# Performance work log

Measured on AMD Instinct MI355X. Metric: run time of the kernel, lower is better.

The kernel has to match this reference:

```python
import jax, jax.numpy as jnp
import numpy as np

EPS = 1e-4
SLOPE = 0.01
NFFT = 512
HOP = 256
CH_IN = 8
CH_H = 64
FREQ = NFFT // 2 + 1
LEN = 48000
BATCH = 2


def hann(n):
    return (0.5 - 0.5 * jnp.cos(2.0 * np.pi * jnp.arange(n) / n)).astype(jnp.float32)


def stft(x):
    # x: (B, C, L) -> (B, 2, C, F, T)  (torch.stft: center=True, reflect pad, hann window)
    pad = NFFT // 2
    xp = jnp.pad(x, ((0, 0), (0, 0), (pad, pad)), mode='reflect')
    T = 1 + x.shape[-1] // HOP
    idx = jnp.arange(T)[:, None] * HOP + jnp.arange(NFFT)[None, :]
    frames = xp[..., idx] * hann(NFFT)            # (B, C, T, NFFT)
    sp = jnp.fft.rfft(frames, axis=-1)            # (B, C, T, F)
    sp = jnp.swapaxes(sp, -1, -2)                 # (B, C, F, T)
    return jnp.stack([sp.real, sp.imag], axis=1).astype(jnp.float32)


def istft(re, im, length):
    # re, im: (B, C, F, T) -> (B, C, length) via windowed overlap-add
    sp = jnp.swapaxes(re + 1j * im, -1, -2)       # (B, C, T, F)
    win = hann(NFFT)
    frames = jnp.fft.irfft(sp, n=NFFT, axis=-1) * win
    pad = NFFT // 2
    total = length + 2 * pad
    T = frames.shape[-2]
    idx = jnp.arange(T)[:, None] * HOP + jnp.arange(NFFT)[None, :]
    out = jnp.zeros(frames.shape[:-2] + (total,), frames.dtype).at[..., idx].add(frames)
    wsum = jnp.zeros((total,), frames.dtype).at[idx].add(jnp.broadcast_to(win ** 2, (T, NFFT)))
    return (out / jnp.maximum(wsum, 1e-11))[..., pad:pad + length]


def conv2d(x, w, b, padT=0):
    y = jax.lax.conv_general_dilated(x, w, (1, 1), ((0, 0), (padT, padT)),
                                     dimension_numbers=('NCHW', 'OIHW', 'NCHW'))
    return y + b[None, :, None, None]


def cconv(x, w, b, padT=0):
    # complex conv on x: (B,2,C,F,T); w: (2,O,C,kf,kt) = [W_real, W_imag]; b: (2,O)
    r = conv2d(x[:, 0], w[0], b[0], padT) - conv2d(x[:, 1], w[1], b[1], padT)
    i = conv2d(x[:, 1], w[0], b[0], padT) + conv2d(x[:, 0], w[1], b[1], padT)
    return jnp.stack([r, i], axis=1)


def modExp(x, m=5.0):
    em = float(np.exp(m))
    return jnp.where(x > m, (x - m) * em + em, jnp.exp(jnp.minimum(x, m)))


def cExp(t):
    e = modExp(t[:, 0]) - 1.0
    return jnp.stack([e * jnp.cos(t[:, 1] - 1.0), e * jnp.sin(t[:, 1] - 1.0)], axis=1)


def snap(x):
    x = jnp.where((x >= 0) & (x < EPS), EPS, x)
    return jnp.where((x < 0) & (x > -EPS), -EPS, x)


def cLog(t):
    re = snap(t[:, 0])
    im = snap(t[:, 1])
    real = jnp.log(jnp.sqrt(im ** 2 + re ** 2 + EPS ** 2) + 1.0)
    imag = jnp.arctan(im / re)
    return jnp.stack([real, imag], axis=1)


def cMul(a, b):
    r = a[:, 0] * b[:, 0] - a[:, 1] * b[:, 1]
    i = a[:, 0] * b[:, 1] + a[:, 1] * b[:, 0]
    return jnp.stack([r, i], axis=1)


def trelu(t, tr, b):
    nr = t[:, 0] * tr[0, 0] + t[:, 1] * tr[0, 1] + b[0]
    ni = t[:, 0] * tr[1, 0] + t[:, 1] * tr[1, 1] + b[1]
    return jnp.stack([jax.nn.leaky_relu(nr, SLOPE), jax.nn.leaky_relu(ni, SLOPE)], axis=1)


def tgate(t, tr, b):
    gr = jax.nn.sigmoid(t[:, 0] * tr[0, 0] + t[:, 1] * tr[0, 1] + b[0])
    gi = jax.nn.sigmoid(t[:, 0] * tr[1, 0] + t[:, 1] * tr[1, 1] + b[1])
    return gr * gi + (1.0 - gr) * (1.0 - gi)


def perm(t):
    return jnp.transpose(t, (0, 1, 3, 2, 4))


def lrelu(x):
    return jax.nn.leaky_relu(x, SLOPE)


def forward(mix, fs_w, fs_b, fr_w, fr_b, c1r_w, c1r_b, c1i_w, c1i_b, c1_w, c1_b,
            c2r_w, c2r_b, c2i_w, c2i_b, c2_w, c2_b, a1_t, a1_b, a2_t, a2_b,
            c3r_w, c3r_b, c3i_w, c3i_b, c3_w, c3_b, c4r_w, c4r_b, c4i_w, c4i_b,
            c4_w, c4_b, a3_t, a3_b, a4_t, a4_b, f1_w, f1_b, f2_w, f2_b,
            cw_w, cw_b, fg_t, fg_b):
    ts = perm(cconv(perm(stft(mix)), fs_w, fs_b))      # (B,2,C,F,T)
    # ---- branch 1 ----
    tl = cLog(ts)
    tl = jnp.stack([conv2d(tl[:, 0], c1r_w, c1r_b), conv2d(tl[:, 1], c1r_w, c1r_b)], 1)
    tl = jnp.stack([conv2d(lrelu(tl[:, 0]), c1i_w, c1i_b), conv2d(tl[:, 1], c1i_w, c1i_b)], 1)
    tl = trelu(cExp(tl), a1_t, a1_b)
    t = cconv(tl, c1_w, c1_b)
    tl = cLog(t)
    tl = jnp.stack([conv2d(tl[:, 0], c2r_w, c2r_b, 7), conv2d(tl[:, 1], c2r_w, c2r_b, 7)], 1)[..., :-7]
    tl = jnp.stack([conv2d(lrelu(tl[:, 0]), c2i_w, c2i_b, 7), conv2d(tl[:, 1], c2i_w, c2i_b, 7)], 1)[..., :-7]
    tl = cExp(tl)
    tl1 = tl
    tc = cconv(ts, c2_w, c2_b, 7)[..., :-7]
    t = trelu(cMul(tl, tc), a2_t, a2_b)
    t = cconv(t, f1_w, f1_b)
    td1 = jnp.sum(ts - t, axis=2, keepdims=True) / ts.shape[2]
    # ---- branch 2 ----
    tl = cLog(ts)
    tl = jnp.stack([conv2d(tl[:, 0], c3r_w, c3r_b), conv2d(tl[:, 1], c3r_w, c3r_b)], 1)
    tl = jnp.stack([conv2d(lrelu(tl[:, 0]), c3i_w, c3i_b), conv2d(tl[:, 1], c3i_w, c3i_b)], 1)
    tl = trelu(cExp(tl), a3_t, a3_b)
    t = cconv(tl, c3_w, c3_b)
    tl = cLog(t)
    tl = jnp.stack([conv2d(tl[:, 0], c4r_w, c4r_b, 7), conv2d(tl[:, 1], c4r_w, c4r_b, 7)], 1)[..., :-7]
    tl = jnp.stack([conv2d(lrelu(tl[:, 0]), c4i_w, c4i_b, 7), conv2d(tl[:, 1], c4i_w, c4i_b, 7)], 1)[..., :-7]
    tl = cExp(tl)
    tc = cconv(ts, c4_w, c4_b, 7)[..., :-7]
    t = trelu(cMul(tl, tc), a4_t, a4_b)
    td2 = cconv(t, f2_w, f2_b)                         # (B,2,1,F,T)
    # ---- fuse ----
    f = cconv(jnp.concatenate([tl1, tl], axis=2), cw_w, cw_b)
    f = tgate(f, fg_t, fg_b)[:, None]                  # (B,1,1,F,T)
    td = td1 * f + td2 * (1.0 - f)
    t = perm(cconv(perm(td), fr_w, fr_b))
    return istft(t[:, 0], t[:, 1], LEN)                # (B,1,LEN)


def setup_inputs() -> dict:
    ks = iter(jax.random.split(jax.random.key(0), 64))
    def rn(shape, s=0.05):
        return s * jax.random.normal(next(ks), shape, jnp.float32)
    F, C, H = FREQ, CH_IN, CH_H
    inp = {
        'mix': jax.random.normal(next(ks), (BATCH, C, LEN), jnp.float32),
        'fs_w': rn((2, F, F, 1, 1)), 'fs_b': rn((2, F), 0.01),
        'fr_w': rn((2, F, F, 1, 1)), 'fr_b': rn((2, F), 0.01),
        'c1r_w': rn((H, C, 1, 1)), 'c1r_b': rn((H,), 0.01),
        'c1i_w': rn((H, H, 1, 1)), 'c1i_b': rn((H,), 0.01),
        'c1_w': rn((2, H, H, 1, 1)), 'c1_b': rn((2, H), 0.01),
        'c2r_w': rn((H, H, 1, 8)), 'c2r_b': rn((H,), 0.01),
        'c2i_w': rn((H, H, 1, 8)), 'c2i_b': rn((H,), 0.01),
        'c2_w': rn((2, H, C, 1, 8)), 'c2_b': rn((2, H), 0.01),
        'a1_t': rn((2, 2, H, F, 1), 0.5), 'a1_b': rn((2, H, F, 1), 0.5),
        'a2_t': rn((2, 2, H, F, 1), 0.5), 'a2_b': rn((2, H, F, 1), 0.5),
        'c3r_w': rn((H, C, 1, 1)), 'c3r_b': rn((H,), 0.01),
        'c3i_w': rn((H, H, 1, 1)), 'c3i_b': rn((H,), 0.01),
        'c3_w': rn((2, H, H, 1, 1)), 'c3_b': rn((2, H), 0.01),
        'c4r_w': rn((H, H, 1, 8)), 'c4r_b': rn((H,), 0.01),
        'c4i_w': rn((H, H, 1, 8)), 'c4i_b': rn((H,), 0.01),
        'c4_w': rn((2, H, C, 1, 8)), 'c4_b': rn((2, H), 0.01),
        'a3_t': rn((2, 2, H, F, 1), 0.5), 'a3_b': rn((2, H, F, 1), 0.5),
        'a4_t': rn((2, 2, H, F, 1), 0.5), 'a4_b': rn((2, H, F, 1), 0.5),
        'f1_w': rn((2, C, H, 1, 1)), 'f1_b': rn((2, C), 0.01),
        'f2_w': rn((2, 1, H, 1, 1)), 'f2_b': rn((2, 1), 0.01),
        'cw_w': rn((2, 1, 2 * H, 1, 1)), 'cw_b': rn((2, 1), 0.01),
        'fg_t': rn((2, 2, 1, F, 1), 0.5), 'fg_b': rn((2, 1, F, 1), 0.5),
    }
    return inp


def reference(mix, fs_w, fs_b, fr_w, fr_b, c1r_w, c1r_b, c1i_w, c1i_b, c1_w, c1_b,
              c2r_w, c2r_b, c2i_w, c2i_b, c2_w, c2_b, a1_t, a1_b, a2_t, a2_b,
              c3r_w, c3r_b, c3i_w, c3i_b, c3_w, c3_b, c4r_w, c4r_b, c4i_w, c4i_b,
              c4_w, c4_b, a3_t, a3_b, a4_t, a4_b, f1_w, f1_b, f2_w, f2_b,
              cw_w, cw_b, fg_t, fg_b):
    return forward(mix, fs_w, fs_b, fr_w, fr_b, c1r_w, c1r_b, c1i_w, c1i_b, c1_w, c1_b,
                   c2r_w, c2r_b, c2i_w, c2i_b, c2_w, c2_b, a1_t, a1_b, a2_t, a2_b,
                   c3r_w, c3r_b, c3i_w, c3i_b, c3_w, c3_b, c4r_w, c4r_b, c4i_w, c4i_b,
                   c4_w, c4_b, a3_t, a3_b, a4_t, a4_b, f1_w, f1_b, f2_w, f2_b,
                   cw_w, cw_b, fg_t, fg_b)
```

## Files before the change

kernel.cpp:

```cpp
#include <hip/hip_runtime.h>
#include <math.h>

#define DEV __device__ __forceinline__

constexpr int B_   = 2;
constexpr int C_IN = 8;
constexpr int H_   = 64;
constexpr int F_   = 257;
constexpr int T_   = 188;
constexpr int TW   = 96;
constexpr int NFFT = 512;
constexpr int HOP  = 256;
constexpr int LEN  = 48000;
constexpr int PADL = 256;
constexpr int FT   = F_ * T_;
constexpr float EPSV  = 1e-4f;
constexpr float SLOPEV = 0.01f;
constexpr float PI2 = 6.283185307179586f;

typedef __attribute__((ext_vector_type(8))) short short8;
typedef __attribute__((ext_vector_type(4))) short short4v;
typedef __attribute__((ext_vector_type(4))) float float4v;

DEV float lrelu_f(float x) { return x > 0.f ? x : SLOPEV * x; }
DEV float snap_f(float x) {
  if (x >= 0.f && x < EPSV) return EPSV;
  if (x < 0.f && x > -EPSV) return -EPSV;
  return x;
}
DEV float fast_atan(float z) {
  float az = fabsf(z);
  float u = az > 1.f ? __builtin_amdgcn_rcpf(az) : az;
  float u2 = u * u;
  float p = -0.01172120f;
  p = p * u2 + 0.05265332f;
  p = p * u2 - 0.11643287f;
  p = p * u2 + 0.19354346f;
  p = p * u2 - 0.33262347f;
  p = p * u2 + 0.99997726f;
  float r = p * u;
  if (az > 1.f) r = 1.5707963267948966f - r;
  return z < 0.f ? -r : r;
}
DEV float modexp_f(float x) {
  const float em = 148.4131591025766f;
  return x > 5.f ? (x - 5.f) * em + em : __expf(x);
}
DEV void cexp_f(float tr, float ti, float& er, float& ei) {
  float e = modexp_f(tr) - 1.f;
  float a = ti - 1.f;
  er = e * __cosf(a); ei = e * __sinf(a);
}
DEV float sigmoid_f(float x) { return 1.f / (1.f + __expf(-x)); }

DEV short f2bf(float x) {
  unsigned u = __float_as_uint(x);
  unsigned r = (u + 0x7fffu + ((u >> 16) & 1u)) >> 16;
  return (short)r;
}
DEV float bf2f(short h) {
  return __uint_as_float(((unsigned)(unsigned short)h) << 16);
}

__global__ void k_mixsplit(const float* __restrict__ x, short* __restrict__ hi,
                           short* __restrict__ lo) {
  int i = blockIdx.x * 256 + threadIdx.x;
  if (i >= B_ * C_IN * LEN / 4) return;
  float4v v = *(const float4v*)(x + (size_t)i * 4);
  short4v h, l;
  #pragma unroll
  for (int j = 0; j < 4; ++j) {
    h[j] = f2bf(v[j]);
    l[j] = f2bf(v[j] - bf2f(h[j]));
  }
  *(short4v*)(hi + (size_t)i * 4) = h;
  *(short4v*)(lo + (size_t)i * 4) = l;
}

__global__ __launch_bounds__(256) void k_mixdft(const float* __restrict__ W,
                                                short* __restrict__ wpk) {
  constexpr int MT = 33;
  __shared__ float wr_s[F_], wi_s[F_];
  int m = blockIdx.x;
  int k = blockIdx.y * 256 + threadIdx.x;
  int po = m >= F_;
  int fo = m - po * F_;
  if (m < 2 * F_) {
    for (int i = threadIdx.x; i < F_; i += 256) {
      wr_s[i] = W[fo * F_ + i];
      wi_s[i] = W[F_ * F_ + fo * F_ + i];
    }
  }
  __syncthreads();
  float val = 0.f;
  if (m < 2 * F_) {
    float sd, cd;
    sincosf((PI2 / NFFT) * k, &sd, &cd);
    float cs = 1.f, sn = 0.f;
    float ar = 0.f, ai = 0.f;
    for (int fi = 0; fi < F_; ++fi) {
      float wrv = wr_s[fi], wiv = wi_s[fi];
      ar += wrv * cs + wiv * sn;
      ai += wiv * cs - wrv * sn;
      float t2 = cs * cd - sn * sd;
      sn = sn * cd + cs * sd;
      cs = t2;
    }
    float win = 0.5f - 0.5f * cd;
    val = (po ? ai : ar) * win;
  }
  int mtg = m >> 4;
  int lane2 = ((k >> 3) & 3) * 16 + (m & 15);
  int s = k >> 5;
  int j = k & 7;
  short hi = f2bf(val);
  short lo = f2bf(val - bf2f(hi));
  wpk[(((0 * 16 + s) * MT + mtg) * 64 + lane2) * 8 + j] = hi;
  wpk[(((16 + s) * MT + mtg) * 64 + lane2) * 8 + j] = lo;
}

constexpr int TWS = 48;
__global__ __launch_bounds__(256) void k_stftmix(
    const short* __restrict__ mhi, const short* __restrict__ mlo,
    const short* __restrict__ wpk, const float* __restrict__ bias,
    float* __restrict__ Y) {
  constexpr int PITCH = 136;
  constexpr int MT = 33;
  __shared__ short xs_hi[TWS * PITCH];
  __shared__ short xs_lo[TWS * PITCH];
  int mg = blockIdx.x;
  int bc = blockIdx.y;
  int b = bc >> 3, c = bc & 7;
  int t0 = blockIdx.z * TWS;
  int tid = threadIdx.x;
  int lane = tid & 63;
  int wv = __builtin_amdgcn_readfirstlane(tid >> 6);
  int mtg = mg * 4 + wv;
  int q = lane >> 4;
  int n = lane & 15;

  const short* mh_ = mhi + (size_t)(b * C_IN + c) * LEN;
  const short* ml_ = mlo + (size_t)(b * C_IN + c) * LEN;

  float4v acc[3];
  #pragma unroll
  for (int nt = 0; nt < 3; ++nt) acc[nt] = (float4v)(0.f);

  const short8* wp = (const short8*)wpk;
  for (int round = 0; round < 4; ++round) {
    if (round) __syncthreads();
    for (int i = tid; i < TWS * 16; i += 256) {
      int tl = i >> 4, u = i & 15;
      int kk0 = u * 8;
      int t = t0 + tl;
      int g0 = t * HOP + round * 128 + kk0 - PADL;
      short8 h, l;
      if (t < T_ && g0 >= 0 && g0 + 7 < LEN) {
        h = *(const short8*)(mh_ + g0);
        l = *(const short8*)(ml_ + g0);
      } else {
        #pragma unroll
        for (int j = 0; j < 8; ++j) {
          short hv = 0, lv = 0;
          if (t < T_) {
            int g = g0 + j;
            if (g < 0) g = -g;
            if (g >= LEN) g = 2 * LEN - 2 - g;
            hv = mh_[g]; lv = ml_[g];
          }
          h[j] = hv; l[j] = lv;
        }
      }
      *(short8*)&xs_hi[tl * PITCH + kk0] = h;
      *(short8*)&xs_lo[tl * PITCH + kk0] = l;
    }
    __syncthreads();
    #pragma unroll
    for (int s2 = 0; s2 < 4; ++s2) {
      int s = round * 4 + s2;
      short8 Ah, Al;
      if (mtg < MT) {
        Ah = wp[((0 * 16 + s) * MT + mtg) * 64 + lane];
        Al = wp[((16 + s) * MT + mtg) * 64 + lane];
      }
      short8 Bh[3], Bl[3];
      #pragma unroll
      for (int nt = 0; nt < 3; ++nt) {
        int off = (nt * 16 + n) * PITCH + s2 * 32 + q * 8;
        Bh[nt] = *(const short8*)&xs_hi[off];
        Bl[nt] = *(const short8*)&xs_lo[off];
      }
      if (mtg < MT) {
        #pragma unroll
        for (int nt = 0; nt < 3; ++nt) {
          acc[nt] = __builtin_amdgcn_mfma_f32_16x16x32_bf16(Ah, Bh[nt], acc[nt], 0, 0, 0);
          acc[nt] = __builtin_amdgcn_mfma_f32_16x16x32_bf16(Ah, Bl[nt], acc[nt], 0, 0, 0);
          acc[nt] = __builtin_amdgcn_mfma_f32_16x16x32_bf16(Al, Bh[nt], acc[nt], 0, 0, 0);
        }
      }
    }
  }

  if (mtg < MT) {
    #pragma unroll
    for (int nt = 0; nt < 3; ++nt) {
      int t = t0 + nt * 16 + n;
      if (t >= T_) continue;
      #pragma unroll
      for (int r = 0; r < 4; ++r) {
        int m = mtg * 16 + q * 4 + r;
        if (m >= 2 * F_) continue;
        int po = m >= F_;
        int fo = m - po * F_;
        float badd = po ? bias[fo] + bias[F_ + fo] : bias[fo] - bias[F_ + fo];
        Y[((size_t)((b * 2 + po) * C_IN + c)) * FT + fo * T_ + t] = acc[nt][r] + badd;
      }
    }
  }
}

template<int CH>
__global__ void k_fmix(const float* __restrict__ X, const float* __restrict__ W,
                       const float* __restrict__ bias, float* __restrict__ Y) {
  int fo = blockIdx.x;
  int bc = blockIdx.y; int c = bc % CH; int b = bc / CH;
  int t = threadIdx.x;
  if (t >= T_) return;
  const float* wr = W + fo * F_;
  const float* wi = W + F_ * F_ + fo * F_;
  const float* xr = X + ((b * 2 + 0) * CH + c) * FT + t;
  const float* xi = X + ((b * 2 + 1) * CH + c) * FT + t;
  float ar = 0.f, ai = 0.f;
  for (int fi = 0; fi < F_; ++fi) {
    float wrv = wr[fi], wiv = wi[fi];
    float xrv = xr[fi * T_], xiv = xi[fi * T_];
    ar += wrv * xrv - wiv * xiv;
    ai += wrv * xiv + wiv * xrv;
  }
  float br = bias[fo], bi = bias[F_ + fo];
  Y[((b * 2 + 0) * CH + c) * FT + fo * T_ + t] = ar + br - bi;
  Y[((b * 2 + 1) * CH + c) * FT + fo * T_ + t] = ai + br + bi;
}

template<int CIN, int K>
DEV void repack_real_body(const float* __restrict__ W, short* __restrict__ wpk, int i) {
  constexpr int CC = (CIN >= 32) ? (CIN / 32) : 1;
  constexpr int NSTEP = (CIN * K + 31) / 32;
  int total = 2 * NSTEP * 4 * 64 * 8;
  if (i >= total) return;
  int j = i & 7;
  int lane = (i >> 3) & 63;
  int mt = (i >> 9) & 3;
  int s = (i >> 11) % NSTEP;
  int split = i / (NSTEP * 2048);
  int q = lane >> 4;
  int m = mt * 16 + (lane & 15);
  int tap = s / CC;
  int c = (s % CC) * 32 + q * 8 + j;
  float w = 0.f;
  if (c < CIN && tap < K) w = W[(m * CIN + c) * K + tap];
  short hi = f2bf(w);
  wpk[i] = split ? f2bf(w - bf2f(hi)) : hi;
}

template<int CIN2, int COUT2, int K>
DEV void repack_cplx_body(const float* __restrict__ W, short* __restrict__ wpk, int i) {
  constexpr int CIN = CIN2 / 2, COUT = COUT2 / 2;
  constexpr int NSTEP = CIN2 * K / 32;
  constexpr int MT = (COUT2 + 15) / 16;
  int total = 2 * NSTEP * MT * 64 * 8;
  if (i >= total) return;
  int j = i & 7;
  int lane = (i >> 3) & 63;
  int idx = i >> 9;
  int mt = idx % MT; idx /= MT;
  int s = idx % NSTEP;
  int split = idx / NSTEP;
  int q = lane >> 4;
  int m = mt * 16 + (lane & 15);
  int tap, pi, ci;
  if constexpr (CIN2 == 128) {
    tap = 0;
    int cs = s * 32 + q * 8 + j;
    int half = cs / 64, r = cs % 64;
    ci = half * 32 + r / 2;
    pi = r & 1;
  } else {
    tap = s * 2 + (q >> 1);
    int cs = (q & 1) * 8 + j;
    pi = cs / CIN;
    ci = cs % CIN;
  }
  float w = 0.f;
  if (m < COUT2) {
    int po = m / COUT, ho = m % COUT;
    float wr = W[((0 * COUT + ho) * CIN + ci) * K + tap];
    float wi = W[((1 * COUT + ho) * CIN + ci) * K + tap];
    w = (po == pi) ? wr : (po == 0 ? -wi : wi);
  }
  short hi = f2bf(w);
  wpk[i] = split ? f2bf(w - bf2f(hi)) : hi;
}

__global__ __launch_bounds__(256) void k_repack_all(
    const float* c1r_w, const float* c1i_w, const float* c2r_w, const float* c2i_w,
    const float* c3r_w, const float* c3i_w, const float* c4r_w, const float* c4i_w,
    const float* c1_w, const float* c2_w, const float* c3_w, const float* c4_w,
    const float* f1_w, const float* f2_w,
    short* o0, short* o1, short* o2, short* o3, short* o4, short* o5, short* o6,
    short* o7, short* o8, short* o9, short* o10, short* o11, short* o12, short* o13) {
  int i = blockIdx.x * 256 + threadIdx.x;
  switch (blockIdx.y) {
    case 0:  repack_real_body<C_IN, 1>(c1r_w, o0, i); break;
    case 1:  repack_real_body<H_,   1>(c1i_w, o1, i); break;
    case 2:  repack_real_body<H_,   8>(c2r_w, o2, i); break;
    case 3:  repack_real_body<H_,   8>(c2i_w, o3, i); break;
    case 4:  repack_real_body<C_IN, 1>(c3r_w, o4, i); break;
    case 5:  repack_real_body<H_,   1>(c3i_w, o5, i); break;
    case 6:  repack_real_body<H_,   8>(c4r_w, o6, i); break;
    case 7:  repack_real_body<H_,   8>(c4i_w, o7, i); break;
    case 8:  repack_cplx_body<128, 128, 1>(c1_w, o8, i); break;
    case 9:  repack_cplx_body<16,  128, 8>(c2_w, o9, i); break;
    case 10: repack_cplx_body<128, 128, 1>(c3_w, o10, i); break;
    case 11: repack_cplx_body<16,  128, 8>(c4_w, o11, i); break;
    case 12: repack_cplx_body<128, 16,  1>(f1_w, o12, i); break;
    case 13: repack_cplx_body<128, 2,   1>(f2_w, o13, i); break;
  }
}

template<int CIN, int K, int PRO>
__global__ __launch_bounds__(256) void k_conv_mfma(
    const float* __restrict__ X, const short* __restrict__ wpk,
    const float* __restrict__ bias, float* __restrict__ Y) {
  constexpr int CC = (CIN >= 32) ? (CIN / 32) : 1;
  constexpr int NSTEP = (CIN * K + 31) / 32;
  constexpr int PITCH = 72;
  constexpr int ROWS = TW + (K - 1);
  __shared__ short xs_hi[ROWS * PITCH];
  __shared__ short xs_lo[ROWS * PITCH];
  int f = blockIdx.x;
  int bp = blockIdx.y; int p = bp & 1; int b = bp >> 1;
  int t0 = blockIdx.z * TW;
  int tid = threadIdx.x;

  for (int i = tid; i < ROWS * PITCH; i += 256) { xs_hi[i] = 0; xs_lo[i] = 0; }
  __syncthreads();

  const float* Xr_ = X + (size_t)((b * 2 + 0) * CIN) * FT + f * T_;
  const float* Xi_ = X + (size_t)((b * 2 + 1) * CIN) * FT + f * T_;
  const float* Xp  = X + (size_t)((b * 2 + p) * CIN) * FT + f * T_;
  for (int i = tid; i < CIN * ROWS; i += 256) {
    int c = i / ROWS, rr = i % ROWS;
    int t = t0 + rr - (K - 1);
    if (t < 0 || t >= T_) continue;
    float v;
    if (PRO == 2) {
      float re = snap_f(Xr_[c * FT + t]);
      float im = snap_f(Xi_[c * FT + t]);
      v = (p == 0) ? __logf(sqrtf(im * im + re * re + EPSV * EPSV) + 1.f)
                   : fast_atan(im / re);
    } else {
      v = Xp[c * FT + t];
      if (PRO == 1 && p == 0) v = lrelu_f(v);
    }
    short hi = f2bf(v);
    short lo = f2bf(v - bf2f(hi));
    xs_hi[rr * PITCH + c] = hi;
    xs_lo[rr * PITCH + c] = lo;
  }
  __syncthreads();

  int lane = tid & 63;
  int wv = __builtin_amdgcn_readfirstlane(tid >> 6);
  int mh = wv >> 1;
  int tc = wv & 1;
  int q = lane >> 4;
  int n = lane & 15;
  int wbase = tc * 48;

  float4v acc[2][3];
  #pragma unroll
  for (int mt = 0; mt < 2; ++mt)
    #pragma unroll
    for (int nt = 0; nt < 3; ++nt) acc[mt][nt] = (float4v)(0.f);

  const short8* wp = (const short8*)wpk;
  #pragma unroll
  for (int s = 0; s < NSTEP; ++s) {
    int tap = s / CC;
    int c0 = (s % CC) * 32;
    short8 Ah[2], Al[2];
    #pragma unroll
    for (int mt = 0; mt < 2; ++mt) {
      int mtg = mh * 2 + mt;
      Ah[mt] = wp[((0 * NSTEP + s) * 4 + mtg) * 64 + lane];
      Al[mt] = wp[((1 * NSTEP + s) * 4 + mtg) * 64 + lane];
    }
    short8 Bh[3], Bl[3];
    #pragma unroll
    for (int nt = 0; nt < 3; ++nt) {
      int off = (wbase + nt * 16 + n + tap) * PITCH + c0 + q * 8;
      Bh[nt] = *(const short8*)&xs_hi[off];
      Bl[nt] = *(const short8*)&xs_lo[off];
    }
    #pragma unroll
    for (int mt = 0; mt < 2; ++mt) {
      #pragma unroll
      for (int nt = 0; nt < 3; ++nt) {
        acc[mt][nt] = __builtin_amdgcn_mfma_f32_16x16x32_bf16(Ah[mt], Bh[nt], acc[mt][nt], 0, 0, 0);
        acc[mt][nt] = __builtin_amdgcn_mfma_f32_16x16x32_bf16(Ah[mt], Bl[nt], acc[mt][nt], 0, 0, 0);
        acc[mt][nt] = __builtin_amdgcn_mfma_f32_16x16x32_bf16(Al[mt], Bh[nt], acc[mt][nt], 0, 0, 0);
      }
    }
  }

  float* Yp = Y + (size_t)((b * 2 + p) * H_) * FT + f * T_;
  #pragma unroll
  for (int nt = 0; nt < 3; ++nt) {
    int t = t0 + wbase + nt * 16 + n;
    if (t >= T_) continue;
    #pragma unroll
    for (int mt = 0; mt < 2; ++mt) {
      #pragma unroll
      for (int r = 0; r < 4; ++r) {
        int h = (mh * 2 + mt) * 16 + q * 4 + r;
        Yp[h * FT + t] = acc[mt][nt][r] + bias[h];
      }
    }
  }
}

template<int COUT2, int PRO>
__global__ __launch_bounds__(256) void k_cconv128(
    const float* __restrict__ X0, const float* __restrict__ X1,
    const short* __restrict__ wpk,
    const float* __restrict__ at, const float* __restrict__ ab,
    const float* __restrict__ bias, float* __restrict__ Y) {
  constexpr int MT = (COUT2 + 15) / 16;
  constexpr int MTW = (MT > 4) ? 4 : MT;
  constexpr int COUT = COUT2 / 2;
  constexpr int NSTEP = 4;
  constexpr int PITCH = 72;
  __shared__ short xs_hi[TW * PITCH];
  __shared__ short xs_lo[TW * PITCH];
  __shared__ float coef[6][64];
  int f = blockIdx.x;
  int b = blockIdx.y;
  int t0 = blockIdx.z * TW;
  int tid = threadIdx.x;
  int lane = tid & 63;
  int wv = __builtin_amdgcn_readfirstlane(tid >> 6);
  int mh = wv >> 1;
  int tc = wv & 1;
  int q = lane >> 4;
  int n = lane & 15;
  int wbase = tc * 48;

  if (tid < 64) {
    int h = tid;
    coef[0][h] = at[(0 * H_ + h) * F_ + f];
    coef[1][h] = at[(1 * H_ + h) * F_ + f];
    coef[2][h] = at[(2 * H_ + h) * F_ + f];
    coef[3][h] = at[(3 * H_ + h) * F_ + f];
    coef[4][h] = ab[h * F_ + f];
    coef[5][h] = ab[(H_ + h) * F_ + f];
  }
  for (int i = tid; i < TW * PITCH; i += 256) { xs_hi[i] = 0; xs_lo[i] = 0; }

  const float* b0r = X0 + (size_t)((b * 2 + 0) * H_) * FT + f * T_;
  const float* b0i = X0 + (size_t)((b * 2 + 1) * H_) * FT + f * T_;
  const float* b1r = X1 + (size_t)((b * 2 + 0) * H_) * FT + f * T_;
  const float* b1i = X1 + (size_t)((b * 2 + 1) * H_) * FT + f * T_;

  float4v acc[MTW][3];
  #pragma unroll
  for (int mt = 0; mt < MTW; ++mt)
    #pragma unroll
    for (int nt = 0; nt < 3; ++nt) acc[mt][nt] = (float4v)(0.f);

  const short8* wp = (const short8*)wpk;
  for (int half = 0; half < 2; ++half) {
    __syncthreads();
    for (int i = tid; i < 32 * TW; i += 256) {
      int hh = i / TW, tl = i % TW;
      int t = t0 + tl;
      if (t >= T_) continue;
      int h = half * 32 + hh;
      float xr = b0r[h * FT + t], xi = b0i[h * FT + t];
      float vr, vi;
      if (PRO == 1) {
        float er, ei;
        cexp_f(xr, xi, er, ei);
        vr = lrelu_f(er * coef[0][h] + ei * coef[1][h] + coef[4][h]);
        vi = lrelu_f(er * coef[2][h] + ei * coef[3][h] + coef[5][h]);
      } else {
        float yr = b1r[h * FT + t], yi = b1i[h * FT + t];
        float mr = xr * yr - xi * yi;
        float mi = xr * yi + xi * yr;
        vr = lrelu_f(mr * coef[0][h] + mi * coef[1][h] + coef[4][h]);
        vi = lrelu_f(mr * coef[2][h] + mi * coef[3][h] + coef[5][h]);
      }
      int cs0 = hh * 2, cs1 = hh * 2 + 1;
      short hr = f2bf(vr), hi2 = f2bf(vi);
      xs_hi[tl * PITCH + cs0] = hr;
      xs_lo[tl * PITCH + cs0] = f2bf(vr - bf2f(hr));
      xs_hi[tl * PITCH + cs1] = hi2;
      xs_lo[tl * PITCH + cs1] = f2bf(vi - bf2f(hi2));
    }
    __syncthreads();
    #pragma unroll
    for (int s2 = 0; s2 < 2; ++s2) {
      int s = half * 2 + s2;
      short8 Bh[3], Bl[3];
      #pragma unroll
      for (int nt = 0; nt < 3; ++nt) {
        int off = (wbase + nt * 16 + n) * PITCH + s2 * 32 + q * 8;
        Bh[nt] = *(const short8*)&xs_hi[off];
        Bl[nt] = *(const short8*)&xs_lo[off];
      }
      #pragma unroll
      for (int mt = 0; mt < MTW; ++mt) {
        int mtg = mh * 4 + mt;
        if (mtg >= MT) continue;
        short8 Ah = wp[((0 * NSTEP + s) * MT + mtg) * 64 + lane];
        short8 Al = wp[((1 * NSTEP + s) * MT + mtg) * 64 + lane];
        #pragma unroll
        for (int nt = 0; nt < 3; ++nt) {
          acc[mt][nt] = __builtin_amdgcn_mfma_f32_16x16x32_bf16(Ah, Bh[nt], acc[mt][nt], 0, 0, 0);
          acc[mt][nt] = __builtin_amdgcn_mfma_f32_16x16x32_bf16(Ah, Bl[nt], acc[mt][nt], 0, 0, 0);
          acc[mt][nt] = __builtin_amdgcn_mfma_f32_16x16x32_bf16(Al, Bh[nt], acc[mt][nt], 0, 0, 0);
        }
      }
    }
  }

  float* Yp = Y + (size_t)b * COUT2 * FT + f * T_;
  #pragma unroll
  for (int nt = 0; nt < 3; ++nt) {
    int t = t0 + wbase + nt * 16 + n;
    if (t >= T_) continue;
    #pragma unroll
    for (int mt = 0; mt < MTW; ++mt) {
      int mtg = mh * 4 + mt;
      if (mtg >= MT) continue;
      #pragma unroll
      for (int r = 0; r < 4; ++r) {
        int o2 = mtg * 16 + q * 4 + r;
        if (o2 >= COUT2) continue;
        int po = o2 / COUT, ho = o2 % COUT;
        float br = bias[ho], bi = bias[COUT + ho];
        float badd = (po == 0) ? br - bi : br + bi;
        Yp[o2 * FT + t] = acc[mt][nt][r] + badd;
      }
    }
  }
}

__global__ __launch_bounds__(256) void k_cconv16(
    const float* __restrict__ X, const short* __restrict__ wpk,
    const float* __restrict__ bias, float* __restrict__ Y) {
  constexpr int MT = 8, NSTEP = 4, PITCH = 24, ROWS = TW + 7, COUT = 64, COUT2 = 128;
  __shared__ short xs_hi[ROWS * PITCH];
  __shared__ short xs_lo[ROWS * PITCH];
  int f = blockIdx.x;
  int b = blockIdx.y;
  int t0 = blockIdx.z * TW;
  int tid = threadIdx.x;

  for (int i = tid; i < ROWS * PITCH; i += 256) { xs_hi[i] = 0; xs_lo[i] = 0; }
  __syncthreads();

  const float* Xp = X + (size_t)b * 16 * FT + f * T_;
  for (int i = tid; i < 16 * ROWS; i += 256) {
    int c = i / ROWS, rr = i % ROWS;
    int t = t0 + rr - 7;
    if (t < 0 || t >= T_) continue;
    float v = Xp[c * FT + t];
    short hi = f2bf(v);
    short lo = f2bf(v - bf2f(hi));
    xs_hi[rr * PITCH + c] = hi;
    xs_lo[rr * PITCH + c] = lo;
  }
  __syncthreads();

  int lane = tid & 63;
  int wv = __builtin_amdgcn_readfirstlane(tid >> 6);
  int mh = wv >> 1;
  int tc = wv & 1;
  int q = lane >> 4;
  int n = lane & 15;
  int wbase = tc * 48;

  float4v acc[4][3];
  #pragma unroll
  for (int mt = 0; mt < 4; ++mt)
    #pragma unroll
    for (int nt = 0; nt < 3; ++nt) acc[mt][nt] = (float4v)(0.f);

  const short8* wp = (const short8*)wpk;
  #pragma unroll
  for (int s = 0; s < NSTEP; ++s) {
    int tap = s * 2 + (q >> 1);
    int coff = (q & 1) * 8;
    short8 Bh[3], Bl[3];
    #pragma unroll
    for (int nt = 0; nt < 3; ++nt) {
      int off = (wbase + nt * 16 + n + tap) * PITCH + coff;
      Bh[nt] = *(const short8*)&xs_hi[off];
      Bl[nt] = *(const short8*)&xs_lo[off];
    }
    #pragma unroll
    for (int mt = 0; mt < 4; ++mt) {
      int mtg = mh * 4 + mt;
      short8 Ah = wp[((0 * NSTEP + s) * MT + mtg) * 64 + lane];
      short8 Al = wp[((1 * NSTEP + s) * MT + mtg) * 64 + lane];
      #pragma unroll
      for (int nt = 0; nt < 3; ++nt) {
        acc[mt][nt] = __builtin_amdgcn_mfma_f32_16x16x32_bf16(Ah, Bh[nt], acc[mt][nt], 0, 0, 0);
        acc[mt][nt] = __builtin_amdgcn_mfma_f32_16x16x32_bf16(Ah, Bl[nt], acc[mt][nt], 0, 0, 0);
        acc[mt][nt] = __builtin_amdgcn_mfma_f32_16x16x32_bf16(Al, Bh[nt], acc[mt][nt], 0, 0, 0);
      }
    }
  }

  float* Yp = Y + (size_t)b * COUT2 * FT + f * T_;
  #pragma unroll
  for (int nt = 0; nt < 3; ++nt) {
    int t = t0 + wbase + nt * 16 + n;
    if (t >= T_) continue;
    #pragma unroll
    for (int mt = 0; mt < 4; ++mt) {
      #pragma unroll
      for (int r = 0; r < 4; ++r) {
        int o2 = (mh * 4 + mt) * 16 + q * 4 + r;
        int po = o2 / COUT, ho = o2 % COUT;
        float br = bias[ho], bi = bias[COUT + ho];
        float badd = (po == 0) ? br - bi : br + bi;
        Yp[o2 * FT + t] = acc[mt][nt][r] + badd;
      }
    }
  }
}

__global__ void k_cexp(const float* __restrict__ X, float* __restrict__ Y) {
  int i = blockIdx.x * blockDim.x + threadIdx.x;
  if (i >= B_ * H_ * FT) return;
  int b = i / (H_ * FT);
  int r = i % (H_ * FT);
  int i0 = (b * 2) * H_ * FT + r;
  int i1 = i0 + H_ * FT;
  float er, ei;
  cexp_f(X[i0], X[i1], er, ei);
  Y[i0] = er;
  Y[i1] = ei;
}

__global__ void k_td1(const float* __restrict__ ts, const float* __restrict__ t8,
                      float* __restrict__ td1) {
  int i = blockIdx.x * blockDim.x + threadIdx.x;
  if (i >= B_ * 2 * FT) return;
  int bp = i / FT; int r = i % FT;
  const float* a = ts + bp * C_IN * FT + r;
  const float* c2 = t8 + bp * C_IN * FT + r;
  float acc = 0.f;
  #pragma unroll
  for (int c = 0; c < C_IN; ++c) acc += a[c * FT] - c2[c * FT];
  td1[i] = acc * (1.f / C_IN);
}

__global__ void k_fuse(const float* __restrict__ tl1, const float* __restrict__ tl2,
                       const float* __restrict__ td1, const float* __restrict__ td2,
                       const float* __restrict__ cw, const float* __restrict__ cwb,
                       const float* __restrict__ fgt, const float* __restrict__ fgb,
                       float* __restrict__ td) {
  int i = blockIdx.x * blockDim.x + threadIdx.x;
  if (i >= B_ * FT) return;
  int b = i / FT; int r = i % FT; int f = r / T_;
  const float* x1r = tl1 + (b * 2) * H_ * FT + r;
  const float* x1i = x1r + H_ * FT;
  const float* x2r = tl2 + (b * 2) * H_ * FT + r;
  const float* x2i = x2r + H_ * FT;
  float fr = 0.f, fi = 0.f;
  for (int c = 0; c < H_; ++c) {
    float w1r = cw[c], w2r = cw[H_ + c], w1i = cw[2 * H_ + c], w2i = cw[3 * H_ + c];
    float a1r = x1r[c * FT], a1i = x1i[c * FT];
    float a2r = x2r[c * FT], a2i = x2i[c * FT];
    fr += w1r * a1r - w1i * a1i + w2r * a2r - w2i * a2i;
    fi += w1r * a1i + w1i * a1r + w2r * a2i + w2i * a2r;
  }
  fr += cwb[0] - cwb[1];
  fi += cwb[0] + cwb[1];
  float t00 = fgt[f], t01 = fgt[F_ + f], t10 = fgt[2 * F_ + f], t11 = fgt[3 * F_ + f];
  float gr = sigmoid_f(fr * t00 + fi * t01 + fgb[f]);
  float gi = sigmoid_f(fr * t10 + fi * t11 + fgb[F_ + f]);
  float gg = gr * gi + (1.f - gr) * (1.f - gi);
  int i0 = (b * 2) * FT + r, i1 = i0 + FT;
  td[i0] = td1[i0] * gg + td2[i0] * (1.f - gg);
  td[i1] = td1[i1] * gg + td2[i1] * (1.f - gg);
}

__global__ __launch_bounds__(320) void k_iframes(const float* __restrict__ sp,
                                                 float* __restrict__ frames) {
  __shared__ float Xr[F_], Xi[F_];
  int blk = blockIdx.x;
  int t = blk % T_;
  int b = blk / T_;
  int tid = threadIdx.x;
  for (int i = tid; i < F_; i += 320) {
    Xr[i] = sp[(b * 2 + 0) * FT + i * T_ + t];
    Xi[i] = sp[(b * 2 + 1) * FT + i * T_ + t];
  }
  __syncthreads();
  int n = tid;
  if (n <= 256) {
    float sd, cd;
    sincosf((PI2 / NFFT) * n, &sd, &cd);
    float cs = cd, sn = sd;
    float ac = 0.f, as = 0.f;
    for (int f = 1; f < 256; ++f) {
      ac += Xr[f] * cs;
      as += Xi[f] * sn;
      float t2 = cs * cd - sn * sd;
      sn = sn * cd + cs * sd;
      cs = t2;
    }
    float base = Xr[0] + Xr[256] * (1.f - 2.f * (n & 1));
    float win = 0.5f - 0.5f * cd;
    float scale = win * (1.f / NFFT);
    float* fr = frames + (size_t)(b * T_ + t) * NFFT;
    fr[n] = (base + 2.f * ac - 2.f * as) * scale;
    if (n >= 1 && n <= 255)
      fr[NFFT - n] = (base + 2.f * ac + 2.f * as) * scale;
  }
}

__global__ void k_ola(const float* __restrict__ frames, float* __restrict__ out) {
  int i = blockIdx.x * blockDim.x + threadIdx.x;
  if (i >= B_ * LEN) return;
  int b = i / LEN; int j = i % LEN;
  int p = j + PADL;
  int t0 = p / HOP; int n0 = p - t0 * HOP;
  float acc = 0.f, wsum = 0.f;
  if (t0 < T_) {
    acc += frames[(b * T_ + t0) * NFFT + n0];
    float w = 0.5f - 0.5f * __cosf((PI2 / NFFT) * n0);
    wsum += w * w;
  }
  int t1 = t0 - 1, n1 = n0 + HOP;
  if (t1 >= 0 && t1 < T_) {
    acc += frames[(b * T_ + t1) * NFFT + n1];
    float w = 0.5f - 0.5f * __cosf((PI2 / NFFT) * n1);
    wsum += w * w;
  }
  out[i] = acc / fmaxf(wsum, 1e-11f);
}

extern "C" void kernel_launch(void* const* d_in, const int* in_sizes, int n_in,
                              void* d_out, int out_size, void* d_ws, size_t ws_size,
                              hipStream_t stream) {
  const float* mix   = (const float*)d_in[0];
  const float* fs_w  = (const float*)d_in[1];
  const float* fs_b  = (const float*)d_in[2];
  const float* fr_w  = (const float*)d_in[3];
  const float* fr_b  = (const float*)d_in[4];
  const float* c1r_w = (const float*)d_in[5];
  const float* c1r_b = (const float*)d_in[6];
  const float* c1i_w = (const float*)d_in[7];
  const float* c1i_b = (const float*)d_in[8];
  const float* c1_w  = (const float*)d_in[9];
  const float* c1_b  = (const float*)d_in[10];
  const float* c2r_w = (const float*)d_in[11];
  const float* c2r_b = (const float*)d_in[12];
  const float* c2i_w = (const float*)d_in[13];
  const float* c2i_b = (const float*)d_in[14];
  const float* c2_w  = (const float*)d_in[15];
  const float* c2_b  = (const float*)d_in[16];
  const float* a1_t  = (const float*)d_in[17];
  const float* a1_b  = (const float*)d_in[18];
  const float* a2_t  = (const float*)d_in[19];
  const float* a2_b  = (const float*)d_in[20];
  const float* c3r_w = (const float*)d_in[21];
  const float* c3r_b = (const float*)d_in[22];
  const float* c3i_w = (const float*)d_in[23];
  const float* c3i_b = (const float*)d_in[24];
  const float* c3_w  = (const float*)d_in[25];
  const float* c3_b  = (const float*)d_in[26];
  const float* c4r_w = (const float*)d_in[27];
  const float* c4r_b = (const float*)d_in[28];
  const float* c4i_w = (const float*)d_in[29];
  const float* c4i_b = (const float*)d_in[30];
  const float* c4_w  = (const float*)d_in[31];
  const float* c4_b  = (const float*)d_in[32];
  const float* a3_t  = (const float*)d_in[33];
  const float* a3_b  = (const float*)d_in[34];
  const float* a4_t  = (const float*)d_in[35];
  const float* a4_b  = (const float*)d_in[36];
  const float* f1_w  = (const float*)d_in[37];
  const float* f1_b  = (const float*)d_in[38];
  const float* f2_w  = (const float*)d_in[39];
  const float* f2_b  = (const float*)d_in[40];
  const float* cw_w  = (const float*)d_in[41];
  const float* cw_b  = (const float*)d_in[42];
  const float* fg_t  = (const float*)d_in[43];
  const float* fg_b  = (const float*)d_in[44];

  const size_t S8 = (size_t)B_ * 2 * C_IN * FT;
  const size_t SH = (size_t)B_ * 2 * H_ * FT;
  const size_t S1 = (size_t)B_ * 2 * FT;
  float* ws  = (float*)d_ws;
  float* ts0 = ws;
  float* ts  = ts0 + S8;
  float* A   = ts + S8;
  float* Bb  = A + SH;
  float* Cc  = Bb + SH;
  float* td1 = Cc + SH;
  float* td2 = td1 + S1;
  float* tdf = td2 + S1;
  float* tdr = tdf + S1;
  float* s8  = ts0;
  float* frames = ts0;

  short* wtail = (short*)(tdr + S1);
  constexpr int SZ_C8K1   = 2 * 1  * 4 * 64 * 8;
  constexpr int SZ_C64K1  = 2 * 2  * 4 * 64 * 8;
  constexpr int SZ_C64K8  = 2 * 16 * 4 * 64 * 8;
  constexpr int SZ_CC128  = 2 * 4  * 8 * 64 * 8;
  constexpr int SZ_CF     = 2 * 4  * 1 * 64 * 8;
  constexpr int SZ_SM     = 2 * 16 * 33 * 64 * 8;
  short* w_c1r = wtail;
  short* w_c1i = w_c1r + SZ_C8K1;
  short* w_c2r = w_c1i + SZ_C64K1;
  short* w_c2i = w_c2r + SZ_C64K8;
  short* w_c3r = w_c2i + SZ_C64K8;
  short* w_c3i = w_c3r + SZ_C8K1;
  short* w_c4r = w_c3i + SZ_C64K1;
  short* w_c4i = w_c4r + SZ_C64K8;
  short* w_cc1 = w_c4i + SZ_C64K8;
  short* w_cc2 = w_cc1 + SZ_CC128;
  short* w_cc3 = w_cc2 + SZ_CC128;
  short* w_cc4 = w_cc3 + SZ_CC128;
  short* w_cf1 = w_cc4 + SZ_CC128;
  short* w_cf2 = w_cf1 + SZ_CF;
  short* w_sm  = w_cf2 + SZ_CF;
  short* mhi   = w_sm + SZ_SM;
  short* mlo   = mhi + (size_t)B_ * C_IN * LEN;

  const int nH = B_ * H_ * FT;
  const int nP = B_ * FT;
  const dim3 rgrid(F_, B_ * 2, 2);
  const dim3 cgrid(F_, B_, 2);

  k_repack_all<<<dim3(256, 14), 256, 0, stream>>>(
      c1r_w, c1i_w, c2r_w, c2i_w, c3r_w, c3i_w, c4r_w, c4i_w,
      c1_w, c2_w, c3_w, c4_w, f1_w, f2_w,
      w_c1r, w_c1i, w_c2r, w_c2i, w_c3r, w_c3i, w_c4r, w_c4i,
      w_cc1, w_cc2, w_cc3, w_cc4, w_cf1, w_cf2);

  k_mixsplit<<<(B_ * C_IN * LEN / 4 + 255) / 256, 256, 0, stream>>>(mix, mhi, mlo);
  k_mixdft<<<dim3(528, 2), 256, 0, stream>>>(fs_w, w_sm);
  k_stftmix<<<dim3(9, 16, 4), 256, 0, stream>>>(mhi, mlo, w_sm, fs_b, ts);

  k_conv_mfma<C_IN, 1, 2><<<rgrid, 256, 0, stream>>>(ts, w_c1r, c1r_b, A);
  k_conv_mfma<H_, 1, 1><<<rgrid, 256, 0, stream>>>(A, w_c1i, c1i_b, Bb);
  k_cconv128<128, 1><<<cgrid, 256, 0, stream>>>(Bb, Bb, w_cc1, a1_t, a1_b, c1_b, A);
  k_conv_mfma<H_, 8, 2><<<rgrid, 256, 0, stream>>>(A, w_c2r, c2r_b, Bb);
  k_conv_mfma<H_, 8, 1><<<rgrid, 256, 0, stream>>>(Bb, w_c2i, c2i_b, A);
  k_cexp<<<(nH + 255) / 256, 256, 0, stream>>>(A, Bb);
  k_cconv16<<<cgrid, 256, 0, stream>>>(ts, w_cc2, c2_b, A);
  k_cconv128<16, 2><<<cgrid, 256, 0, stream>>>(Bb, A, w_cf1, a2_t, a2_b, f1_b, s8);
  k_td1<<<(B_ * 2 * FT + 255) / 256, 256, 0, stream>>>(ts, s8, td1);

  k_conv_mfma<C_IN, 1, 2><<<rgrid, 256, 0, stream>>>(ts, w_c3r, c3r_b, A);
  k_conv_mfma<H_, 1, 1><<<rgrid, 256, 0, stream>>>(A, w_c3i, c3i_b, Cc);
  k_cconv128<128, 1><<<cgrid, 256, 0, stream>>>(Cc, Cc, w_cc3, a3_t, a3_b, c3_b, A);
  k_conv_mfma<H_, 8, 2><<<rgrid, 256, 0, stream>>>(A, w_c4r, c4r_b, Cc);
  k_conv_mfma<H_, 8, 1><<<rgrid, 256, 0, stream>>>(Cc, w_c4i, c4i_b, A);
  k_cexp<<<(nH + 255) / 256, 256, 0, stream>>>(A, Cc);
  k_cconv16<<<cgrid, 256, 0, stream>>>(ts, w_cc4, c4_b, A);
  k_cconv128<2, 2><<<cgrid, 256, 0, stream>>>(Cc, A, w_cf2, a4_t, a4_b, f2_b, td2);

  k_fuse<<<(nP + 255) / 256, 256, 0, stream>>>(Bb, Cc, td1, td2, cw_w, cw_b, fg_t, fg_b, tdf);
  k_fmix<1><<<dim3(F_, B_), 192, 0, stream>>>(tdf, fr_w, fr_b, tdr);
  k_iframes<<<B_ * T_, 320, 0, stream>>>(tdr, frames);
  k_ola<<<(B_ * LEN + 255) / 256, 256, 0, stream>>>(frames, (float*)d_out);
}
```

Before: 846.1 us.

## Swizzle LDS tiles and pass pre-split bf16 hi/lo activations between conv stages

Adds an XOR swizzle to the LDS staging layout in the STFT, 64-channel conv and cconv128 kernels so that the B-fragment short8 reads fall into fewer shared-memory bank conflicts. The conv epilogue can now write packed bf16 hi/lo pairs, with the leaky ReLU folded in. The following conv and the cexp kernel read those pairs directly instead of recomputing the split from fp32, and the prologue index loop drops its per-element division and modulo. In exchange the intermediate buffers change format between stages. The cexp input is now rebuilt from hi+lo, which loses a little precision compared with the original fp32 value.

```diff
diff --git a/kernel.cpp b/kernel.cpp
--- a/kernel.cpp
+++ b/kernel.cpp
@@ -60,6 +60,11 @@
 }
 DEV float bf2f(short h) {
   return __uint_as_float(((unsigned)(unsigned short)h) << 16);
+}
+DEV unsigned pack_hl(float v) {
+  short hi = f2bf(v);
+  short lo = f2bf(v - bf2f(hi));
+  return ((unsigned)(unsigned short)hi << 16) | (unsigned)(unsigned short)lo;
 }
 
 __global__ void k_mixsplit(const float* __restrict__ x, short* __restrict__ hi,
@@ -171,8 +176,9 @@
           h[j] = hv; l[j] = lv;
         }
       }
-      *(short8*)&xs_hi[tl * PITCH + kk0] = h;
-      *(short8*)&xs_lo[tl * PITCH + kk0] = l;
+      int kk0s = kk0 ^ ((tl & 7) << 3);
+      *(short8*)&xs_hi[tl * PITCH + kk0s] = h;
+      *(short8*)&xs_lo[tl * PITCH + kk0s] = l;
     }
     __syncthreads();
     #pragma unroll
@@ -186,7 +192,8 @@
       short8 Bh[3], Bl[3];
       #pragma unroll
       for (int nt = 0; nt < 3; ++nt) {
-        int off = (nt * 16 + n) * PITCH + s2 * 32 + q * 8;
+        int row = nt * 16 + n;
+        int off = row * PITCH + ((s2 * 32 + q * 8) ^ ((row & 7) << 3));
         Bh[nt] = *(const short8*)&xs_hi[off];
         Bl[nt] = *(const short8*)&xs_lo[off];
       }
@@ -328,7 +335,7 @@
   }
 }
 
-template<int CIN, int K, int PRO>
+template<int CIN, int K, int PRO, int EPI>
 __global__ __launch_bounds__(256) void k_conv_mfma(
     const float* __restrict__ X, const short* __restrict__ wpk,
     const float* __restrict__ bias, float* __restrict__ Y) {
@@ -336,6 +343,7 @@
   constexpr int NSTEP = (CIN * K + 31) / 32;
   constexpr int PITCH = 72;
   constexpr int ROWS = TW + (K - 1);
+  constexpr bool SWZ = (CIN == 64);
   __shared__ short xs_hi[ROWS * PITCH];
   __shared__ short xs_lo[ROWS * PITCH];
   int f = blockIdx.x;
@@ -349,24 +357,40 @@
   const float* Xr_ = X + (size_t)((b * 2 + 0) * CIN) * FT + f * T_;
   const float* Xi_ = X + (size_t)((b * 2 + 1) * CIN) * FT + f * T_;
   const float* Xp  = X + (size_t)((b * 2 + p) * CIN) * FT + f * T_;
-  for (int i = tid; i < CIN * ROWS; i += 256) {
-    int c = i / ROWS, rr = i % ROWS;
-    int t = t0 + rr - (K - 1);
-    if (t < 0 || t >= T_) continue;
-    float v;
-    if (PRO == 2) {
-      float re = snap_f(Xr_[c * FT + t]);
-      float im = snap_f(Xi_[c * FT + t]);
-      v = (p == 0) ? __logf(sqrtf(im * im + re * re + EPSV * EPSV) + 1.f)
-                   : fast_atan(im / re);
-    } else {
-      v = Xp[c * FT + t];
-      if (PRO == 1 && p == 0) v = lrelu_f(v);
-    }
-    short hi = f2bf(v);
-    short lo = f2bf(v - bf2f(hi));
-    xs_hi[rr * PITCH + c] = hi;
-    xs_lo[rr * PITCH + c] = lo;
+  const unsigned* Xu = (const unsigned*)X + (size_t)((b * 2 + p) * CIN) * FT + f * T_;
+  {
+    constexpr int STEP_C = 256 / ROWS, STEP_R = 256 % ROWS;
+    int c = tid / ROWS;
+    int rr = tid - c * ROWS;
+    while (c < CIN) {
+      int t = t0 + rr - (K - 1);
+      if (t >= 0 && t < T_) {
+        short hi, lo;
+        if (PRO == 3) {
+          unsigned v = Xu[c * FT + t];
+          hi = (short)(v >> 16);
+          lo = (short)(v & 0xffffu);
+        } else {
+          float v;
+          if (PRO == 2) {
+            float re = snap_f(Xr_[c * FT + t]);
+            float im = snap_f(Xi_[c * FT + t]);
+            v = (p == 0) ? __logf(sqrtf(im * im + re * re + EPSV * EPSV) + 1.f)
+                         : fast_atan(im / re);
+          } else {
+            v = Xp[c * FT + t];
+            if (PRO == 1 && p == 0) v = lrelu_f(v);
+          }
+          hi = f2bf(v);
+          lo = f2bf(v - bf2f(hi));
+        }
+        int sc = SWZ ? (c ^ ((rr & 7) << 3)) : c;
+        xs_hi[rr * PITCH + sc] = hi;
+        xs_lo[rr * PITCH + sc] = lo;
+      }
+      rr += STEP_R; c += STEP_C;
+      if (rr >= ROWS) { rr -= ROWS; c += 1; }
+    }
   }
   __syncthreads();
 
@@ -399,7 +423,10 @@
     short8 Bh[3], Bl[3];
     #pragma unroll
     for (int nt = 0; nt < 3; ++nt) {
-      int off = (wbase + nt * 16 + n + tap) * PITCH + c0 + q * 8;
+      int row = wbase + nt * 16 + n + tap;
+      int colS = c0 + q * 8;
+      if (SWZ) colS ^= (row & 7) << 3;
+      int off = row * PITCH + colS;
       Bh[nt] = *(const short8*)&xs_hi[off];
       Bl[nt] = *(const short8*)&xs_lo[off];
     }
@@ -415,6 +442,7 @@
   }
 
   float* Yp = Y + (size_t)((b * 2 + p) * H_) * FT + f * T_;
+  unsigned* Yu = (unsigned*)Y + (size_t)((b * 2 + p) * H_) * FT + f * T_;
   #pragma unroll
   for (int nt = 0; nt < 3; ++nt) {
     int t = t0 + wbase + nt * 16 + n;
@@ -424,7 +452,13 @@
       #pragma unroll
       for (int r = 0; r < 4; ++r) {
         int h = (mh * 2 + mt) * 16 + q * 4 + r;
-        Yp[h * FT + t] = acc[mt][nt][r] + bias[h];
+        float v = acc[mt][nt][r] + bias[h];
+        if (EPI == 0) {
+          Yp[h * FT + t] = v;
+        } else {
+          if (EPI == 1 && p == 0) v = lrelu_f(v);
+          Yu[h * FT + t] = pack_hl(v);
+        }
       }
     }
   }
@@ -500,7 +534,8 @@
         vr = lrelu_f(mr * coef[0][h] + mi * coef[1][h] + coef[4][h]);
         vi = lrelu_f(mr * coef[2][h] + mi * coef[3][h] + coef[5][h]);
       }
-      int cs0 = hh * 2, cs1 = hh * 2 + 1;
+      int swz = (tl & 7) << 3;
+      int cs0 = (hh * 2) ^ swz, cs1 = (hh * 2 + 1) ^ swz;
       short hr = f2bf(vr), hi2 = f2bf(vi);
       xs_hi[tl * PITCH + cs0] = hr;
       xs_lo[tl * PITCH + cs0] = f2bf(vr - bf2f(hr));
@@ -514,7 +549,8 @@
       short8 Bh[3], Bl[3];
       #pragma unroll
       for (int nt = 0; nt < 3; ++nt) {
-        int off = (wbase + nt * 16 + n) * PITCH + s2 * 32 + q * 8;
+        int row = wbase + nt * 16 + n;
+        int off = row * PITCH + ((s2 * 32 + q * 8) ^ ((row & 7) << 3));
         Bh[nt] = *(const short8*)&xs_hi[off];
         Bl[nt] = *(const short8*)&xs_lo[off];
       }
@@ -642,15 +678,18 @@
   }
 }
 
-__global__ void k_cexp(const float* __restrict__ X, float* __restrict__ Y) {
+__global__ void k_cexp_pk(const unsigned* __restrict__ X, float* __restrict__ Y) {
   int i = blockIdx.x * blockDim.x + threadIdx.x;
   if (i >= B_ * H_ * FT) return;
   int b = i / (H_ * FT);
   int r = i % (H_ * FT);
-  int i0 = (b * 2) * H_ * FT + r;
-  int i1 = i0 + H_ * FT;
+  size_t i0 = (size_t)(b * 2) * H_ * FT + r;
+  size_t i1 = i0 + (size_t)H_ * FT;
+  unsigned v0 = X[i0], v1 = X[i1];
+  float tr = bf2f((short)(v0 >> 16)) + bf2f((short)(v0 & 0xffffu));
+  float ti = bf2f((short)(v1 >> 16)) + bf2f((short)(v1 & 0xffffu));
   float er, ei;
-  cexp_f(X[i0], X[i1], er, ei);
+  cexp_f(tr, ti, er, ei);
   Y[i0] = er;
   Y[i1] = ei;
 }
@@ -860,22 +899,22 @@
   k_mixdft<<<dim3(528, 2), 256, 0, stream>>>(fs_w, w_sm);
   k_stftmix<<<dim3(9, 16, 4), 256, 0, stream>>>(mhi, mlo, w_sm, fs_b, ts);
 
-  k_conv_mfma<C_IN, 1, 2><<<rgrid, 256, 0, stream>>>(ts, w_c1r, c1r_b, A);
-  k_conv_mfma<H_, 1, 1><<<rgrid, 256, 0, stream>>>(A, w_c1i, c1i_b, Bb);
+  k_conv_mfma<C_IN, 1, 2, 1><<<rgrid, 256, 0, stream>>>(ts, w_c1r, c1r_b, A);
+  k_conv_mfma<H_, 1, 3, 0><<<rgrid, 256, 0, stream>>>(A, w_c1i, c1i_b, Bb);
   k_cconv128<128, 1><<<cgrid, 256, 0, stream>>>(Bb, Bb, w_cc1, a1_t, a1_b, c1_b, A);
-  k_conv_mfma<H_, 8, 2><<<rgrid, 256, 0, stream>>>(A, w_c2r, c2r_b, Bb);
-  k_conv_mfma<H_, 8, 1><<<rgrid, 256, 0, stream>>>(Bb, w_c2i, c2i_b, A);
-  k_cexp<<<(nH + 255) / 256, 256, 0, stream>>>(A, Bb);
+  k_conv_mfma<H_, 8, 2, 1><<<rgrid, 256, 0, stream>>>(A, w_c2r, c2r_b, Bb);
+  k_conv_mfma<H_, 8, 3, 2><<<rgrid, 256, 0, stream>>>(Bb, w_c2i, c2i_b, A);
+  k_cexp_pk<<<(nH + 255) / 256, 256, 0, stream>>>((const unsigned*)A, Bb);
   k_cconv16<<<cgrid, 256, 0, stream>>>(ts, w_cc2, c2_b, A);
   k_cconv128<16, 2><<<cgrid, 256, 0, stream>>>(Bb, A, w_cf1, a2_t, a2_b, f1_b, s8);
   k_td1<<<(B_ * 2 * FT + 255) / 256, 256, 0, stream>>>(ts, s8, td1);
 
-  k_conv_mfma<C_IN, 1, 2><<<rgrid, 256, 0, stream>>>(ts, w_c3r, c3r_b, A);
-  k_conv_mfma<H_, 1, 1><<<rgrid, 256, 0, stream>>>(A, w_c3i, c3i_b, Cc);
+  k_conv_mfma<C_IN, 1, 2, 1><<<rgrid, 256, 0, stream>>>(ts, w_c3r, c3r_b, A);
+  k_conv_mfma<H_, 1, 3, 0><<<rgrid, 256, 0, stream>>>(A, w_c3i, c3i_b, Cc);
   k_cconv128<128, 1><<<cgrid, 256, 0, stream>>>(Cc, Cc, w_cc3, a3_t, a3_b, c3_b, A);
-  k_conv_mfma<H_, 8, 2><<<rgrid, 256, 0, stream>>>(A, w_c4r, c4r_b, Cc);
-  k_conv_mfma<H_, 8, 1><<<rgrid, 256, 0, stream>>>(Cc, w_c4i, c4i_b, A);
-  k_cexp<<<(nH + 255) / 256, 256, 0, stream>>>(A, Cc);
+  k_conv_mfma<H_, 8, 2, 1><<<rgrid, 256, 0, stream>>>(A, w_c4r, c4r_b, Cc);
+  k_conv_mfma<H_, 8, 3, 2><<<rgrid, 256, 0, stream>>>(Cc, w_c4i, c4i_b, A);
+  k_cexp_pk<<<(nH + 255) / 256, 256, 0, stream>>>((const unsigned*)A, Cc);
   k_cconv16<<<cgrid, 256, 0, stream>>>(ts, w_cc4, c4_b, A);
   k_cconv128<2, 2><<<cgrid, 256, 0, stream>>>(Cc, A, w_cf2, a4_t, a4_b, f2_b, td2);
 
```

New measurement: 924.8 us. +9.3%, slower.
